# Kernel tuning notes

Measured on AMD Instinct MI355X. Metric: run time of the kernel, lower is better.

## Reference

```python
import jax, jax.numpy as jnp
import numpy as np

B, T, L, H, I, W_OUT = 64, 512, 2, 512, 128, 32


def setup_inputs() -> dict:
    key = jax.random.key(0)
    ks = jax.random.split(key, 12)
    stdv = 1.0 / np.sqrt(H)
    u = lambda k, shape: jax.random.uniform(k, shape, jnp.float32, -stdv, stdv)
    return {
        "x": jax.random.normal(ks[0], (B, T, I), jnp.float32),
        "noise": jax.random.normal(ks[1], (B, T, L, H), jnp.float32) * 0.1,
        "W_ih0": u(ks[2], (H, I)),
        "W_ih1": u(ks[3], (H, H)),
        "W_hh0": u(ks[4], (H, H)),
        "W_hh1": u(ks[5], (H, H)),
        "b_ih0": u(ks[6], (H,)),
        "b_ih1": u(ks[7], (H,)),
        "b_hh0": u(ks[8], (H,)),
        "b_hh1": u(ks[9], (H,)),
        "fc_w": u(ks[10], (W_OUT, H)),
        "fc_b": u(ks[11], (W_OUT,)),
    }


def reference(x, noise, W_ih0, W_ih1, W_hh0, W_hh1, b_ih0, b_ih1, b_hh0, b_hh1, fc_w, fc_b):
    # Sequential two-layer tanh RNN; scan over time keeps hidden state resident.
    h0 = jnp.zeros((B, H), x.dtype)
    h1 = jnp.zeros((B, H), x.dtype)

    def step(carry, inp):
        h0, h1 = carry
        x_t, n_t = inp  # x_t: [B,I], n_t: [B,L,H]
        h0 = jnp.tanh(x_t @ W_ih0.T + b_ih0 + h0 @ W_hh0.T + b_hh0 + n_t[:, 0, :])
        h1 = jnp.tanh(h0 @ W_ih1.T + b_ih1 + h1 @ W_hh1.T + b_hh1 + n_t[:, 1, :])
        return (h0, h1), None

    # time-major scan inputs
    (h0, h1), _ = jax.lax.scan(step, (h0, h1), (jnp.swapaxes(x, 0, 1), jnp.swapaxes(noise, 0, 1)))
    return h1 @ fc_w.T + fc_b  # [B, wheel_len]
```

## Files before the change

### kernel.cpp

```cpp
#include <hip/hip_runtime.h>


#define T_STEPS 512
#define NBATCH  64
#define DRING   256
#define THR_LEAD 192

typedef _Float16 half2v __attribute__((ext_vector_type(2)));

__device__ __forceinline__ unsigned pack2(float a, float b) {
    _Float16 fa = (_Float16)a, fb = (_Float16)b;
    unsigned short ua = __builtin_bit_cast(unsigned short, fa);
    unsigned short ub = __builtin_bit_cast(unsigned short, fb);
    return (unsigned)ua | ((unsigned)ub << 16);
}

__device__ __forceinline__ float dot2acc(unsigned w, unsigned h, float acc) {
#if __has_builtin(__builtin_amdgcn_fdot2)
    return __builtin_amdgcn_fdot2(__builtin_bit_cast(half2v, w),
                                  __builtin_bit_cast(half2v, h), acc, false);
#else
    half2v wv = __builtin_bit_cast(half2v, w);
    half2v hv = __builtin_bit_cast(half2v, h);
    acc = fmaf((float)wv.x, (float)hv.x, acc);
    return fmaf((float)wv.y, (float)hv.y, acc);
#endif
}

__device__ __forceinline__ float fast_tanh(float xv) {
    float e2 = __builtin_amdgcn_exp2f(xv * 2.885390082f);
    return 1.f - 2.f * __builtin_amdgcn_rcpf(e2 + 1.f);
}

__device__ __forceinline__ void bar_lgkm() {
    asm volatile("s_waitcnt lgkmcnt(0)\n\ts_barrier" ::: "memory");
}

__device__ __forceinline__ unsigned poll1(unsigned long long* p, unsigned tag,
                                          long& budget) {
    unsigned long long v = __hip_atomic_load(p, __ATOMIC_RELAXED, __HIP_MEMORY_SCOPE_AGENT);
    while ((unsigned)(v >> 32) != tag && budget > 0) {
        v = __hip_atomic_load(p, __ATOMIC_RELAXED, __HIP_MEMORY_SCOPE_AGENT);
        --budget;
    }
    return (unsigned)v;
}

#define NW0 (4 * 10 * 64 * 64)
#define NW1 (4 * 16 * 64 * 64)

__global__ void init_pack(const float* __restrict__ Wih0, const float* __restrict__ Whh0,
                          const float* __restrict__ Wih1, const float* __restrict__ Whh1,
                          unsigned* __restrict__ wp0, unsigned* __restrict__ wp1,
                          int* __restrict__ prog) {
    int gid = blockIdx.x * 256 + threadIdx.x;
    if (gid == 32) prog[32] = prog[32] + 1;
    if (gid < 32) prog[gid] = 0;
    if (gid < NW0) {
        int lane = gid & 63, slot = (gid >> 6) & 63, t12 = gid >> 12;
        int cs = t12 % 10, s = t12 / 10;
        int rr = slot >> 5, j = slot & 31;
        int r = s * 128 + 2 * lane + rr;
        float w0, w1;
        if (cs < 6)      { int m = cs * 32 + j; int p0 = (m < s * 64) ? m : m + 64;
                           w0 = Whh0[r * 512 + 2 * p0]; w1 = Whh0[r * 512 + 2 * p0 + 1]; }
        else if (cs < 8) { int p0 = s * 64 + (cs - 6) * 32 + j;
                           w0 = Whh0[r * 512 + 2 * p0]; w1 = Whh0[r * 512 + 2 * p0 + 1]; }
        else             { int px = (cs - 8) * 32 + j;
                           w0 = Wih0[r * 128 + 2 * px]; w1 = Wih0[r * 128 + 2 * px + 1]; }
        wp0[gid] = pack2(w0, w1);
    } else if (gid < NW0 + NW1) {
        int g2 = gid - NW0;
        int lane = g2 & 63, slot = (g2 >> 6) & 63, w = (g2 >> 12) & 15, s = g2 >> 16;
        int rr = slot >> 5, j = slot & 31;
        int r = s * 128 + 2 * lane + rr;
        float w0, w1;
        if (w < 8)       { int p = w * 32 + j;
                           w0 = Wih1[r * 512 + 2 * p]; w1 = Wih1[r * 512 + 2 * p + 1]; }
        else if (w < 10) { int p1 = s * 64 + (w - 8) * 32 + j;
                           w0 = Whh1[r * 512 + 2 * p1]; w1 = Whh1[r * 512 + 2 * p1 + 1]; }
        else             { int m = (w - 10) * 32 + j; int p1 = (m < s * 64) ? m : m + 64;
                           w0 = Whh1[r * 512 + 2 * p1]; w1 = Whh1[r * 512 + 2 * p1 + 1]; }
        wp1[g2] = pack2(w0, w1);
    }
}

template <int LAYER>
__device__ __forceinline__ void run_layer(
    int b0, int s, int L, int pair,
    const float* __restrict__ x, const float* __restrict__ noise,
    const unsigned* __restrict__ wp,
    const float* __restrict__ bih, const float* __restrict__ bhh,
    unsigned long long* __restrict__ hb0, unsigned long long* __restrict__ hb1,
    int* __restrict__ prog,
    const float* __restrict__ fcw, const float* __restrict__ fcb,
    float* __restrict__ out) {
    const int w = L >> 6, lane = L & 63;
    const unsigned tagbase = ((unsigned)prog[32]) << 10;
    long budget = 2000000000L;

    int wbase;
    if constexpr (LAYER == 0) { int cs = (w < 12) ? (w >> 1) : (w - 6); wbase = (s * 10 + cs) * 64; }
    else                      { wbase = (s * 16 + w) * 64; }
    unsigned wreg[64];
#pragma unroll
    for (int i = 0; i < 64; ++i) {
        wreg[i] = wp[(size_t)(wbase + i) * 64 + lane];
        asm volatile("" : "+v"(wreg[i]));
    }

    __shared__ float psum[16][2][128];
    __shared__ __align__(16) unsigned priv[16][64];
    __shared__ __align__(16) unsigned hown[128];
    for (int i = L; i < 16 * 64; i += 1024) ((unsigned*)priv)[i] = 0u;
    if (L < 128) hown[L] = 0u;

    const bool isRed = (L < 256);
    const int bbr = L >> 7, rw = L & 127;
    const int rgl = s * 128 + rw;
    float cb = 0.f, nz = 0.f;
    if (isRed) {
        cb = bih[rgl] + bhh[rgl];
        nz = noise[(((size_t)(b0 + bbr) * T_STEPS + 0) * 2 + LAYER) * 512 + rgl];
    }
    __syncthreads();

    unsigned long long pf = 0;
    unsigned long long pfR = 0;
    float2 xf = make_float2(0.f, 0.f);
    if constexpr (LAYER == 1) {
        if (w < 8) {
            unsigned v = poll1(&hb0[((size_t)0 * NBATCH + (b0 + (lane >> 5))) * 256 +
                                    (w * 32 + (lane & 31))], tagbase + 1, budget);
            pf = ((unsigned long long)(tagbase + 1) << 32) | v;
        }
    } else {
        if (w >= 14) {
            int j = lane & 31, bbl = lane >> 5;
            int px = (w - 14) * 32 + j;
            xf = *(const float2*)(x + ((size_t)(b0 + bbl) * T_STEPS + 0) * 128 + 2 * px);
        }
    }

    int known = 0;

    for (int t = 0; t < T_STEPS; ++t) {
        const bool last = (t == T_STEPS - 1);
        __builtin_amdgcn_s_setprio(1);

        if constexpr (LAYER == 1) {
            if (w < 8) {
                const int j = lane & 31, bbl = lane >> 5;
                unsigned want = tagbase + (unsigned)t + 1;
                if ((unsigned)(pf >> 32) != want) {
                    __builtin_amdgcn_s_setprio(0);
                    unsigned v = poll1(&hb0[((size_t)(t & (DRING - 1)) * NBATCH + (b0 + bbl)) * 256 +
                                            (w * 32 + j)], want, budget);
                    pf = ((unsigned long long)want << 32) | v;
                    __builtin_amdgcn_s_setprio(1);
                }
                priv[w][j * 2 + bbl] = (unsigned)pf;
                if (!last)
                    pf = __hip_atomic_load(&hb0[((size_t)((t + 1) & (DRING - 1)) * NBATCH +
                                                 (b0 + bbl)) * 256 + (w * 32 + j)],
                                           __ATOMIC_RELAXED, __HIP_MEMORY_SCOPE_AGENT);
            } else if (w >= 10) {
                if (t > 0) {
                    const int j = lane & 31, bbl = lane >> 5;
                    int m = (w - 10) * 32 + j;
                    int p2 = (m < s * 64) ? m : m + 64;
                    unsigned want = tagbase + (unsigned)t;
                    unsigned v;
                    if ((unsigned)(pfR >> 32) == want) {
                        v = (unsigned)pfR;
                    } else {
                        __builtin_amdgcn_s_setprio(0);
                        v = poll1(&hb1[((size_t)((t - 1) & 3) * NBATCH + (b0 + bbl)) * 256 + p2],
                                  want, budget);
                        __builtin_amdgcn_s_setprio(1);
                    }
                    priv[w][j * 2 + bbl] = v;
                }
            }
        } else {
            if (w < 12) {
                if (t > 0 && lane < 32) {
                    int q = w >> 1, bbw = w & 1;
                    int m = q * 32 + lane;
                    int p2 = (m < s * 64) ? m : m + 64;
                    unsigned want = tagbase + (unsigned)t;
                    unsigned v;
                    if ((unsigned)(pfR >> 32) == want) {
                        v = (unsigned)pfR;
                    } else {
                        __builtin_amdgcn_s_setprio(0);
                        v = poll1(&hb0[((size_t)((t - 1) & (DRING - 1)) * NBATCH +
                                        (b0 + bbw)) * 256 + p2],
                                  want, budget);
                        __builtin_amdgcn_s_setprio(1);
                    }
                    priv[w][lane] = v;
                }
            } else if (w >= 14) {
                const int j = lane & 31, bbl = lane >> 5;
                priv[w][j * 2 + bbl] = pack2(xf.x, xf.y);
                if (!last) {
                    int px = (w - 14) * 32 + j;
                    xf = *(const float2*)(x + ((size_t)(b0 + bbl) * T_STEPS + (t + 1)) * 128 + 2 * px);
                }
            }
        }

        float nznext = 0.f;
        if (!last && isRed)
            nznext = noise[(((size_t)(b0 + bbr) * T_STEPS + (t + 1)) * 2 + LAYER) * 512 + rgl];

        if constexpr (LAYER == 0) {
            if (w < 12) {
                const int q = w >> 1, bbw = w & 1;
                const uint4* hq = (const uint4*)&priv[w][0];
                float ax[2] = {0.f, 0.f}, ay[2] = {0.f, 0.f};
#pragma unroll
                for (int k = 0; k < 8; ++k) {
                    uint4 v = hq[k];
#pragma unroll
                    for (int r2 = 0; r2 < 2; ++r2) {
                        ax[r2] = dot2acc(wreg[r2 * 32 + 4 * k + 0], v.x, ax[r2]);
                        ay[r2] = dot2acc(wreg[r2 * 32 + 4 * k + 1], v.y, ay[r2]);
                        ax[r2] = dot2acc(wreg[r2 * 32 + 4 * k + 2], v.z, ax[r2]);
                        ay[r2] = dot2acc(wreg[r2 * 32 + 4 * k + 3], v.w, ay[r2]);
                    }
                }
                *(float2*)&psum[q][bbw][2 * lane] =
                    make_float2(ax[0] + ay[0], ax[1] + ay[1]);
            } else {
                const uint4* hq = (w < 14) ? (const uint4*)&hown[(w - 12) * 64]
                                           : (const uint4*)&priv[w][0];
                const int pidx = (w < 14) ? (6 + (w - 12)) : (8 + (w - 14));
                float a[2][2] = {{0.f, 0.f}, {0.f, 0.f}};
                float b2[2][2] = {{0.f, 0.f}, {0.f, 0.f}};
#pragma unroll
                for (int k = 0; k < 16; ++k) {
                    uint4 v = hq[k];
                    const int j0 = 2 * k, j1 = 2 * k + 1;
#pragma unroll
                    for (int r2 = 0; r2 < 2; ++r2) {
                        a[r2][0]  = dot2acc(wreg[r2 * 32 + j0], v.x, a[r2][0]);
                        a[r2][1]  = dot2acc(wreg[r2 * 32 + j0], v.y, a[r2][1]);
                        b2[r2][0] = dot2acc(wreg[r2 * 32 + j1], v.z, b2[r2][0]);
                        b2[r2][1] = dot2acc(wreg[r2 * 32 + j1], v.w, b2[r2][1]);
                    }
                }
#pragma unroll
                for (int bb2 = 0; bb2 < 2; ++bb2)
                    *(float2*)&psum[pidx][bb2][2 * lane] =
                        make_float2(a[0][bb2] + b2[0][bb2], a[1][bb2] + b2[1][bb2]);
            }
        } else {
            const uint4* hq = (w == 8 || w == 9) ? (const uint4*)&hown[(w - 8) * 64]
                                                 : (const uint4*)&priv[w][0];
            float a[2][2] = {{0.f, 0.f}, {0.f, 0.f}};
            float b2[2][2] = {{0.f, 0.f}, {0.f, 0.f}};
#pragma unroll
            for (int k = 0; k < 16; ++k) {
                uint4 v = hq[k];
                const int j0 = 2 * k, j1 = 2 * k + 1;
#pragma unroll
                for (int r2 = 0; r2 < 2; ++r2) {
                    a[r2][0]  = dot2acc(wreg[r2 * 32 + j0], v.x, a[r2][0]);
                    a[r2][1]  = dot2acc(wreg[r2 * 32 + j0], v.y, a[r2][1]);
                    b2[r2][0] = dot2acc(wreg[r2 * 32 + j1], v.z, b2[r2][0]);
                    b2[r2][1] = dot2acc(wreg[r2 * 32 + j1], v.w, b2[r2][1]);
                }
            }
#pragma unroll
            for (int bb2 = 0; bb2 < 2; ++bb2)
                *(float2*)&psum[w][bb2][2 * lane] =
                    make_float2(a[0][bb2] + b2[0][bb2], a[1][bb2] + b2[1][bb2]);
        }

        bar_lgkm();

        if (isRed) {
            constexpr int NCH = (LAYER == 0) ? 10 : 16;
            float sum = 0.f;
#pragma unroll
            for (int ch = 0; ch < NCH; ++ch) sum += psum[ch][bbr][rw];
            float h = fast_tanh(sum + cb + nz);
            float hnb = __shfl_down(h, 1);
            if ((L & 1) == 0) {
                unsigned pv = pack2(h, hnb);
                int pr = s * 64 + (rw >> 1);
                unsigned long long atom =
                    ((unsigned long long)(tagbase + (unsigned)t + 1) << 32) |
                    (unsigned long long)pv;
                if constexpr (LAYER == 0) {
                    if (t - known > THR_LEAD) {
                        __builtin_amdgcn_s_setprio(0);
                        while (t - known > THR_LEAD && budget > 0) {
                            known = __hip_atomic_load(&prog[pair], __ATOMIC_RELAXED,
                                                      __HIP_MEMORY_SCOPE_AGENT);
                            --budget;
                        }
                        __builtin_amdgcn_s_setprio(1);
                    }
                    __hip_atomic_store(&hb0[((size_t)(t & (DRING - 1)) * NBATCH + (b0 + bbr)) * 256 + pr],
                                       atom, __ATOMIC_RELAXED, __HIP_MEMORY_SCOPE_AGENT);
                } else {
                    __hip_atomic_store(&hb1[((size_t)(t & 3) * NBATCH + (b0 + bbr)) * 256 + pr],
                                       atom, __ATOMIC_RELAXED, __HIP_MEMORY_SCOPE_AGENT);
                }
                hown[(rw >> 1) * 2 + bbr] = pv;
            }
            nz = nznext;
        }
        if constexpr (LAYER == 1) {
            if (s == 0 && L == 960 && t > 1)
                __hip_atomic_store(&prog[pair], t - 2, __ATOMIC_RELAXED,
                                   __HIP_MEMORY_SCOPE_AGENT);
        }
        bar_lgkm();
        __builtin_amdgcn_s_setprio(0);

        if (!last) {
            if constexpr (LAYER == 1) {
                if (w >= 10) {
                    const int j = lane & 31, bbl = lane >> 5;
                    int m = (w - 10) * 32 + j;
                    int p2 = (m < s * 64) ? m : m + 64;
                    pfR = __hip_atomic_load(&hb1[((size_t)(t & 3) * NBATCH + (b0 + bbl)) * 256 + p2],
                                            __ATOMIC_RELAXED, __HIP_MEMORY_SCOPE_AGENT);
                }
            } else {
                if (w < 12 && lane < 32) {
                    int q = w >> 1, bbw = w & 1;
                    int m = q * 32 + lane;
                    int p2 = (m < s * 64) ? m : m + 64;
                    pfR = __hip_atomic_load(&hb0[((size_t)(t & (DRING - 1)) * NBATCH +
                                                  (b0 + bbw)) * 256 + p2],
                                            __ATOMIC_RELAXED, __HIP_MEMORY_SCOPE_AGENT);
                }
            }
        }
    }

    if constexpr (LAYER == 1) {
        if (s == 0) {
            __shared__ float hs[2][512];
            __shared__ float part[2][512];
            if (L < 512) {
                int bl = L >> 8, pr = L & 255;
                unsigned v = poll1(&hb1[((size_t)((T_STEPS - 1) & 3) * NBATCH + (b0 + bl)) * 256 + pr],
                                   tagbase + (unsigned)T_STEPS, budget);
                half2v h2 = __builtin_bit_cast(half2v, v);
                hs[bl][2 * pr] = (float)h2.x; hs[bl][2 * pr + 1] = (float)h2.y;
            }
            __syncthreads();
            {
                int bl = L >> 9, rest = L & 511, o = rest & 31, seg = rest >> 5;
                const float* wr = fcw + o * 512 + seg * 32;
                const float* hr = &hs[bl][seg * 32];
                float a = 0.f;
#pragma unroll
                for (int k = 0; k < 32; ++k) a = fmaf(wr[k], hr[k], a);
                part[bl][rest] = a;
            }
            __syncthreads();
            if (L < 64) {
                int bl = L >> 5, o = L & 31;
                float ssum = fcb[o];
#pragma unroll
                for (int sgi = 0; sgi < 16; ++sgi) ssum += part[bl][sgi * 32 + o];
                out[(b0 + bl) * 32 + o] = ssum;
            }
        }
    }
}

__global__ __launch_bounds__(1024, 4)
void rnn_dual(const float* __restrict__ x, const float* __restrict__ noise,
              const unsigned* __restrict__ wp0, const unsigned* __restrict__ wp1,
              const float* __restrict__ bih0, const float* __restrict__ bhh0,
              const float* __restrict__ bih1, const float* __restrict__ bhh1,
              const float* __restrict__ fcw, const float* __restrict__ fcb,
              unsigned long long* __restrict__ hb0,
              unsigned long long* __restrict__ hb1,
              int* __restrict__ prog,
              float* __restrict__ out) {
    const int L = threadIdx.x;
    const int gid = blockIdx.x;
    const int cl = gid & 63;
    const int s = gid >> 6;
    const int layer = cl >> 5;
    const int pair = cl & 31;
    const int b0 = pair * 2;
    if (layer == 0)
        run_layer<0>(b0, s, L, pair, x, noise, wp0, bih0, bhh0,
                     hb0, hb1, prog, nullptr, nullptr, nullptr);
    else
        run_layer<1>(b0, s, L, pair, x, noise, wp1, bih1, bhh1,
                     hb0, hb1, prog, fcw, fcb, out);
}

extern "C" void kernel_launch(void* const* d_in, const int* in_sizes, int n_in,
                              void* d_out, int out_size, void* d_ws, size_t ws_size,
                              hipStream_t stream) {
    const float* x     = (const float*)d_in[0];
    const float* noise = (const float*)d_in[1];
    const float* Wih0  = (const float*)d_in[2];
    const float* Wih1  = (const float*)d_in[3];
    const float* Whh0  = (const float*)d_in[4];
    const float* Whh1  = (const float*)d_in[5];
    const float* bih0  = (const float*)d_in[6];
    const float* bih1  = (const float*)d_in[7];
    const float* bhh0  = (const float*)d_in[8];
    const float* bhh1  = (const float*)d_in[9];
    const float* fcw   = (const float*)d_in[10];
    const float* fcb   = (const float*)d_in[11];
    float* out = (float*)d_out;

    char* ws = (char*)d_ws;
    size_t o = 0;
    unsigned* wp0 = (unsigned*)(ws + o); o += (size_t)NW0 * 4;
    unsigned* wp1 = (unsigned*)(ws + o); o += (size_t)NW1 * 4;
    unsigned long long* hb0 = (unsigned long long*)(ws + o);
    o += (size_t)DRING * NBATCH * 256 * 8;
    unsigned long long* hb1 = (unsigned long long*)(ws + o);
    o += (size_t)4 * NBATCH * 256 * 8;
    int* prog = (int*)(ws + o); o += 33 * sizeof(int);

    const int total = NW0 + NW1;
    init_pack<<<(total + 255) / 256, 256, 0, stream>>>(Wih0, Whh0, Wih1, Whh1,
                                                       wp0, wp1, prog);
    rnn_dual<<<256, 1024, 0, stream>>>(x, noise, wp0, wp1, bih0, bhh0, bih1, bhh1,
                                       fcw, fcb, hb0, hb1, prog, out);
}
```

Before: 1.118 ms.

## Replace per-step fdot2 matvec with MFMA 16x16x32 f16 on register-resident weights

The per-timestep recurrent matvec moves from scalar fdot2 dot products over private LDS slices to MFMA 16x16x32 f16 instructions, with weights repacked into MFMA A-fragments held in registers. The hidden state is placed in a double-buffered flat LDS layout that serves as the B operand. The batch of 2 is padded into the 16-wide N dimension, and the per-wave partial sums are reduced in LDS. Double buffering lets the trailing barrier of each step be dropped. The cost is wasted MFMA columns, since only 2 of 16 are real, and an extra barrier between the MFMA and reduction phases.

```diff
diff --git a/kernel.cpp b/kernel.cpp
--- a/kernel.cpp
+++ b/kernel.cpp
@@ -7,6 +7,8 @@
 #define THR_LEAD 192
 
 typedef _Float16 half2v __attribute__((ext_vector_type(2)));
+typedef _Float16 f16x8  __attribute__((ext_vector_type(8)));
+typedef float    f32x4  __attribute__((ext_vector_type(4)));
 
 __device__ __forceinline__ unsigned pack2(float a, float b) {
     _Float16 fa = (_Float16)a, fb = (_Float16)b;
@@ -15,21 +17,14 @@
     return (unsigned)ua | ((unsigned)ub << 16);
 }
 
-__device__ __forceinline__ float dot2acc(unsigned w, unsigned h, float acc) {
-#if __has_builtin(__builtin_amdgcn_fdot2)
-    return __builtin_amdgcn_fdot2(__builtin_bit_cast(half2v, w),
-                                  __builtin_bit_cast(half2v, h), acc, false);
-#else
-    half2v wv = __builtin_bit_cast(half2v, w);
-    half2v hv = __builtin_bit_cast(half2v, h);
-    acc = fmaf((float)wv.x, (float)hv.x, acc);
-    return fmaf((float)wv.y, (float)hv.y, acc);
-#endif
-}
-
 __device__ __forceinline__ float fast_tanh(float xv) {
     float e2 = __builtin_amdgcn_exp2f(xv * 2.885390082f);
     return 1.f - 2.f * __builtin_amdgcn_rcpf(e2 + 1.f);
+}
+
+__device__ __forceinline__ f32x4 mfma16(uint4 a, uint4 b, f32x4 c) {
+    return __builtin_amdgcn_mfma_f32_16x16x32_f16(
+        __builtin_bit_cast(f16x8, a), __builtin_bit_cast(f16x8, b), c, 0, 0, 0);
 }
 
 __device__ __forceinline__ void bar_lgkm() {
@@ -46,42 +41,50 @@
     return (unsigned)v;
 }
 
-#define NW0 (4 * 10 * 64 * 64)
-#define NW1 (4 * 16 * 64 * 64)
+#define NWPF (4 * 16 * 16 * 64)
 
 __global__ void init_pack(const float* __restrict__ Wih0, const float* __restrict__ Whh0,
                           const float* __restrict__ Wih1, const float* __restrict__ Whh1,
-                          unsigned* __restrict__ wp0, unsigned* __restrict__ wp1,
+                          uint4* __restrict__ wp0, uint4* __restrict__ wp1,
                           int* __restrict__ prog) {
     int gid = blockIdx.x * 256 + threadIdx.x;
     if (gid == 32) prog[32] = prog[32] + 1;
     if (gid < 32) prog[gid] = 0;
-    if (gid < NW0) {
-        int lane = gid & 63, slot = (gid >> 6) & 63, t12 = gid >> 12;
-        int cs = t12 % 10, s = t12 / 10;
-        int rr = slot >> 5, j = slot & 31;
-        int r = s * 128 + 2 * lane + rr;
-        float w0, w1;
-        if (cs < 6)      { int m = cs * 32 + j; int p0 = (m < s * 64) ? m : m + 64;
-                           w0 = Whh0[r * 512 + 2 * p0]; w1 = Whh0[r * 512 + 2 * p0 + 1]; }
-        else if (cs < 8) { int p0 = s * 64 + (cs - 6) * 32 + j;
-                           w0 = Whh0[r * 512 + 2 * p0]; w1 = Whh0[r * 512 + 2 * p0 + 1]; }
-        else             { int px = (cs - 8) * 32 + j;
-                           w0 = Wih0[r * 128 + 2 * px]; w1 = Wih0[r * 128 + 2 * px + 1]; }
-        wp0[gid] = pack2(w0, w1);
-    } else if (gid < NW0 + NW1) {
-        int g2 = gid - NW0;
-        int lane = g2 & 63, slot = (g2 >> 6) & 63, w = (g2 >> 12) & 15, s = g2 >> 16;
-        int rr = slot >> 5, j = slot & 31;
-        int r = s * 128 + 2 * lane + rr;
-        float w0, w1;
-        if (w < 8)       { int p = w * 32 + j;
-                           w0 = Wih1[r * 512 + 2 * p]; w1 = Wih1[r * 512 + 2 * p + 1]; }
-        else if (w < 10) { int p1 = s * 64 + (w - 8) * 32 + j;
-                           w0 = Whh1[r * 512 + 2 * p1]; w1 = Whh1[r * 512 + 2 * p1 + 1]; }
-        else             { int m = (w - 10) * 32 + j; int p1 = (m < s * 64) ? m : m + 64;
-                           w0 = Whh1[r * 512 + 2 * p1]; w1 = Whh1[r * 512 + 2 * p1 + 1]; }
-        wp1[g2] = pack2(w0, w1);
+    if (gid < NWPF) {
+        int lane = gid & 63, f = (gid >> 6) & 15, w = (gid >> 10) & 15, s = gid >> 14;
+        uint4 o = make_uint4(0, 0, 0, 0);
+        if (f < 10) {
+            int kc = w >> 2, rg = w & 3, j = f / 5, ktl = f % 5;
+            int r = s * 128 + (rg * 2 + j) * 16 + (lane & 15);
+            unsigned dv[4];
+#pragma unroll
+            for (int d = 0; d < 4; ++d) {
+                int kp = kc * 80 + ktl * 16 + ((lane >> 4) * 4) + d;
+                float w0, w1;
+                if (kp < 64) { w0 = Wih0[r * 128 + 2 * kp]; w1 = Wih0[r * 128 + 2 * kp + 1]; }
+                else { int p0 = kp - 64;
+                       w0 = Whh0[r * 512 + 2 * p0]; w1 = Whh0[r * 512 + 2 * p0 + 1]; }
+                dv[d] = pack2(w0, w1);
+            }
+            o = make_uint4(dv[0], dv[1], dv[2], dv[3]);
+        }
+        wp0[gid] = o;
+    } else if (gid < 2 * NWPF) {
+        int idx = gid - NWPF;
+        int lane = idx & 63, f = (idx >> 6) & 15, w = (idx >> 10) & 15, s = idx >> 14;
+        int kc = w >> 1, rg = w & 1, j = f >> 2, ktl = f & 3;
+        int r = s * 128 + (rg * 4 + j) * 16 + (lane & 15);
+        unsigned dv[4];
+#pragma unroll
+        for (int d = 0; d < 4; ++d) {
+            int kp = kc * 64 + ktl * 16 + ((lane >> 4) * 4) + d;
+            float w0, w1;
+            if (kp < 256) { w0 = Wih1[r * 512 + 2 * kp]; w1 = Wih1[r * 512 + 2 * kp + 1]; }
+            else { int p1 = kp - 256;
+                   w0 = Whh1[r * 512 + 2 * p1]; w1 = Whh1[r * 512 + 2 * p1 + 1]; }
+            dv[d] = pack2(w0, w1);
+        }
+        wp1[idx] = make_uint4(dv[0], dv[1], dv[2], dv[3]);
     }
 }
 
@@ -89,31 +92,34 @@
 __device__ __forceinline__ void run_layer(
     int b0, int s, int L, int pair,
     const float* __restrict__ x, const float* __restrict__ noise,
-    const unsigned* __restrict__ wp,
+    const uint4* __restrict__ wp,
     const float* __restrict__ bih, const float* __restrict__ bhh,
     unsigned long long* __restrict__ hb0, unsigned long long* __restrict__ hb1,
     int* __restrict__ prog,
     const float* __restrict__ fcw, const float* __restrict__ fcb,
     float* __restrict__ out) {
+    constexpr int KC    = (LAYER == 0) ? 4 : 8;
+    constexpr int KT    = (LAYER == 0) ? 5 : 4;
+    constexpr int RT    = (LAYER == 0) ? 2 : 4;
+    constexpr int NPAIR = (LAYER == 0) ? 320 : 512;
+    constexpr int OWNB  = (LAYER == 0) ? 64 : 256;
+    constexpr int NF    = (LAYER == 0) ? 10 : 16;
+    constexpr int KCP   = (LAYER == 0) ? 80 : 64;
+
     const int w = L >> 6, lane = L & 63;
     const unsigned tagbase = ((unsigned)prog[32]) << 10;
     long budget = 2000000000L;
 
-    int wbase;
-    if constexpr (LAYER == 0) { int cs = (w < 12) ? (w >> 1) : (w - 6); wbase = (s * 10 + cs) * 64; }
-    else                      { wbase = (s * 16 + w) * 64; }
-    unsigned wreg[64];
-#pragma unroll
-    for (int i = 0; i < 64; ++i) {
-        wreg[i] = wp[(size_t)(wbase + i) * 64 + lane];
-        asm volatile("" : "+v"(wreg[i]));
-    }
-
-    __shared__ float psum[16][2][128];
-    __shared__ __align__(16) unsigned priv[16][64];
-    __shared__ __align__(16) unsigned hown[128];
-    for (int i = L; i < 16 * 64; i += 1024) ((unsigned*)priv)[i] = 0u;
-    if (L < 128) hown[L] = 0u;
+    uint4 wfr[NF];
+#pragma unroll
+    for (int f = 0; f < NF; ++f) {
+        wfr[f] = wp[(size_t)(((s * 16 + w) * 16) + f) * 64 + lane];
+        asm volatile("" : "+v"(wfr[f].x), "+v"(wfr[f].y), "+v"(wfr[f].z), "+v"(wfr[f].w));
+    }
+
+    __shared__ __align__(16) unsigned hflat[2][2][NPAIR];
+    __shared__ __align__(16) float psum[2][KC][2][128];
+    for (int i = L; i < 2 * 2 * NPAIR; i += 1024) ((unsigned*)hflat)[i] = 0u;
 
     const bool isRed = (L < 256);
     const int bbr = L >> 7, rw = L & 127;
@@ -128,23 +134,20 @@
     unsigned long long pf = 0;
     unsigned long long pfR = 0;
     float2 xf = make_float2(0.f, 0.f);
-    if constexpr (LAYER == 1) {
-        if (w < 8) {
-            unsigned v = poll1(&hb0[((size_t)0 * NBATCH + (b0 + (lane >> 5))) * 256 +
-                                    (w * 32 + (lane & 31))], tagbase + 1, budget);
-            pf = ((unsigned long long)(tagbase + 1) << 32) | v;
-        }
-    } else {
+    if constexpr (LAYER == 0) {
         if (w >= 14) {
-            int j = lane & 31, bbl = lane >> 5;
-            int px = (w - 14) * 32 + j;
+            int j = lane & 31, bbl = lane >> 5, px = (w - 14) * 32 + j;
             xf = *(const float2*)(x + ((size_t)(b0 + bbl) * T_STEPS + 0) * 128 + 2 * px);
         }
     }
 
     int known = 0;
+    const int colm = lane & 15, kg = lane >> 4;
+    const int kcv = (LAYER == 0) ? (w >> 2) : (w >> 1);
+    const int rg  = (LAYER == 0) ? (w & 3)  : (w & 1);
 
     for (int t = 0; t < T_STEPS; ++t) {
+        const int p = t & 1;
         const bool last = (t == T_STEPS - 1);
         __builtin_amdgcn_s_setprio(1);
 
@@ -159,7 +162,7 @@
                     pf = ((unsigned long long)want << 32) | v;
                     __builtin_amdgcn_s_setprio(1);
                 }
-                priv[w][j * 2 + bbl] = (unsigned)pf;
+                hflat[p][bbl][w * 32 + j] = (unsigned)pf;
                 if (!last)
                     pf = __hip_atomic_load(&hb0[((size_t)((t + 1) & (DRING - 1)) * NBATCH +
                                                  (b0 + bbl)) * 256 + (w * 32 + j)],
@@ -171,43 +174,40 @@
                     int p2 = (m < s * 64) ? m : m + 64;
                     unsigned want = tagbase + (unsigned)t;
                     unsigned v;
-                    if ((unsigned)(pfR >> 32) == want) {
-                        v = (unsigned)pfR;
-                    } else {
+                    if ((unsigned)(pfR >> 32) == want) v = (unsigned)pfR;
+                    else {
                         __builtin_amdgcn_s_setprio(0);
                         v = poll1(&hb1[((size_t)((t - 1) & 3) * NBATCH + (b0 + bbl)) * 256 + p2],
                                   want, budget);
                         __builtin_amdgcn_s_setprio(1);
                     }
-                    priv[w][j * 2 + bbl] = v;
+                    hflat[p][bbl][256 + p2] = v;
                 }
             }
         } else {
-            if (w < 12) {
-                if (t > 0 && lane < 32) {
-                    int q = w >> 1, bbw = w & 1;
-                    int m = q * 32 + lane;
+            if (w >= 8 && w < 14) {
+                if (t > 0) {
+                    int idx = (w - 8) * 64 + lane;
+                    int bbl = (idx >= 192) ? 1 : 0;
+                    int m = idx - bbl * 192;
                     int p2 = (m < s * 64) ? m : m + 64;
                     unsigned want = tagbase + (unsigned)t;
                     unsigned v;
-                    if ((unsigned)(pfR >> 32) == want) {
-                        v = (unsigned)pfR;
-                    } else {
+                    if ((unsigned)(pfR >> 32) == want) v = (unsigned)pfR;
+                    else {
                         __builtin_amdgcn_s_setprio(0);
                         v = poll1(&hb0[((size_t)((t - 1) & (DRING - 1)) * NBATCH +
-                                        (b0 + bbw)) * 256 + p2],
+                                        (b0 + bbl)) * 256 + p2],
                                   want, budget);
                         __builtin_amdgcn_s_setprio(1);
                     }
-                    priv[w][lane] = v;
+                    hflat[p][bbl][64 + p2] = v;
                 }
             } else if (w >= 14) {
-                const int j = lane & 31, bbl = lane >> 5;
-                priv[w][j * 2 + bbl] = pack2(xf.x, xf.y);
-                if (!last) {
-                    int px = (w - 14) * 32 + j;
+                const int j = lane & 31, bbl = lane >> 5, px = (w - 14) * 32 + j;
+                hflat[p][bbl][px] = pack2(xf.x, xf.y);
+                if (!last)
                     xf = *(const float2*)(x + ((size_t)(b0 + bbl) * T_STEPS + (t + 1)) * 128 + 2 * px);
-                }
             }
         }
 
@@ -215,77 +215,31 @@
         if (!last && isRed)
             nznext = noise[(((size_t)(b0 + bbr) * T_STEPS + (t + 1)) * 2 + LAYER) * 512 + rgl];
 
-        if constexpr (LAYER == 0) {
-            if (w < 12) {
-                const int q = w >> 1, bbw = w & 1;
-                const uint4* hq = (const uint4*)&priv[w][0];
-                float ax[2] = {0.f, 0.f}, ay[2] = {0.f, 0.f};
-#pragma unroll
-                for (int k = 0; k < 8; ++k) {
-                    uint4 v = hq[k];
-#pragma unroll
-                    for (int r2 = 0; r2 < 2; ++r2) {
-                        ax[r2] = dot2acc(wreg[r2 * 32 + 4 * k + 0], v.x, ax[r2]);
-                        ay[r2] = dot2acc(wreg[r2 * 32 + 4 * k + 1], v.y, ay[r2]);
-                        ax[r2] = dot2acc(wreg[r2 * 32 + 4 * k + 2], v.z, ax[r2]);
-                        ay[r2] = dot2acc(wreg[r2 * 32 + 4 * k + 3], v.w, ay[r2]);
-                    }
-                }
-                *(float2*)&psum[q][bbw][2 * lane] =
-                    make_float2(ax[0] + ay[0], ax[1] + ay[1]);
-            } else {
-                const uint4* hq = (w < 14) ? (const uint4*)&hown[(w - 12) * 64]
-                                           : (const uint4*)&priv[w][0];
-                const int pidx = (w < 14) ? (6 + (w - 12)) : (8 + (w - 14));
-                float a[2][2] = {{0.f, 0.f}, {0.f, 0.f}};
-                float b2[2][2] = {{0.f, 0.f}, {0.f, 0.f}};
-#pragma unroll
-                for (int k = 0; k < 16; ++k) {
-                    uint4 v = hq[k];
-                    const int j0 = 2 * k, j1 = 2 * k + 1;
-#pragma unroll
-                    for (int r2 = 0; r2 < 2; ++r2) {
-                        a[r2][0]  = dot2acc(wreg[r2 * 32 + j0], v.x, a[r2][0]);
-                        a[r2][1]  = dot2acc(wreg[r2 * 32 + j0], v.y, a[r2][1]);
-                        b2[r2][0] = dot2acc(wreg[r2 * 32 + j1], v.z, b2[r2][0]);
-                        b2[r2][1] = dot2acc(wreg[r2 * 32 + j1], v.w, b2[r2][1]);
-                    }
-                }
-#pragma unroll
-                for (int bb2 = 0; bb2 < 2; ++bb2)
-                    *(float2*)&psum[pidx][bb2][2 * lane] =
-                        make_float2(a[0][bb2] + b2[0][bb2], a[1][bb2] + b2[1][bb2]);
-            }
-        } else {
-            const uint4* hq = (w == 8 || w == 9) ? (const uint4*)&hown[(w - 8) * 64]
-                                                 : (const uint4*)&priv[w][0];
-            float a[2][2] = {{0.f, 0.f}, {0.f, 0.f}};
-            float b2[2][2] = {{0.f, 0.f}, {0.f, 0.f}};
-#pragma unroll
-            for (int k = 0; k < 16; ++k) {
-                uint4 v = hq[k];
-                const int j0 = 2 * k, j1 = 2 * k + 1;
-#pragma unroll
-                for (int r2 = 0; r2 < 2; ++r2) {
-                    a[r2][0]  = dot2acc(wreg[r2 * 32 + j0], v.x, a[r2][0]);
-                    a[r2][1]  = dot2acc(wreg[r2 * 32 + j0], v.y, a[r2][1]);
-                    b2[r2][0] = dot2acc(wreg[r2 * 32 + j1], v.z, b2[r2][0]);
-                    b2[r2][1] = dot2acc(wreg[r2 * 32 + j1], v.w, b2[r2][1]);
-                }
-            }
-#pragma unroll
-            for (int bb2 = 0; bb2 < 2; ++bb2)
-                *(float2*)&psum[w][bb2][2 * lane] =
-                    make_float2(a[0][bb2] + b2[0][bb2], a[1][bb2] + b2[1][bb2]);
-        }
-
         bar_lgkm();
 
+        {
+            uint4 Bfr[KT];
+            const unsigned* hbase = &hflat[p][colm & 1][kcv * KCP + kg * 4];
+#pragma unroll
+            for (int ktl = 0; ktl < KT; ++ktl)
+                Bfr[ktl] = *(const uint4*)&hbase[ktl * 16];
+#pragma unroll
+            for (int j = 0; j < RT; ++j) {
+                f32x4 C = {0.f, 0.f, 0.f, 0.f};
+#pragma unroll
+                for (int ktl = 0; ktl < KT; ++ktl)
+                    C = mfma16(wfr[j * KT + ktl], Bfr[ktl], C);
+                if (colm < 2)
+                    *(f32x4*)&psum[p][kcv][colm][(rg * RT + j) * 16 + 4 * kg] = C;
+            }
+        }
+
+        bar_lgkm();
+
         if (isRed) {
-            constexpr int NCH = (LAYER == 0) ? 10 : 16;
             float sum = 0.f;
 #pragma unroll
-            for (int ch = 0; ch < NCH; ++ch) sum += psum[ch][bbr][rw];
+            for (int c2 = 0; c2 < KC; ++c2) sum += psum[p][c2][bbr][rw];
             float h = fast_tanh(sum + cb + nz);
             float hnb = __shfl_down(h, 1);
             if ((L & 1) == 0) {
@@ -310,7 +264,7 @@
                     __hip_atomic_store(&hb1[((size_t)(t & 3) * NBATCH + (b0 + bbr)) * 256 + pr],
                                        atom, __ATOMIC_RELAXED, __HIP_MEMORY_SCOPE_AGENT);
                 }
-                hown[(rw >> 1) * 2 + bbr] = pv;
+                hflat[p ^ 1][bbr][OWNB + s * 64 + (rw >> 1)] = pv;
             }
             nz = nznext;
         }
@@ -319,7 +273,6 @@
                 __hip_atomic_store(&prog[pair], t - 2, __ATOMIC_RELAXED,
                                    __HIP_MEMORY_SCOPE_AGENT);
         }
-        bar_lgkm();
         __builtin_amdgcn_s_setprio(0);
 
         if (!last) {
@@ -332,12 +285,13 @@
                                             __ATOMIC_RELAXED, __HIP_MEMORY_SCOPE_AGENT);
                 }
             } else {
-                if (w < 12 && lane < 32) {
-                    int q = w >> 1, bbw = w & 1;
-                    int m = q * 32 + lane;
+                if (w >= 8 && w < 14) {
+                    int idx = (w - 8) * 64 + lane;
+                    int bbl = (idx >= 192) ? 1 : 0;
+                    int m = idx - bbl * 192;
                     int p2 = (m < s * 64) ? m : m + 64;
                     pfR = __hip_atomic_load(&hb0[((size_t)(t & (DRING - 1)) * NBATCH +
-                                                  (b0 + bbw)) * 256 + p2],
+                                                  (b0 + bbl)) * 256 + p2],
                                             __ATOMIC_RELAXED, __HIP_MEMORY_SCOPE_AGENT);
                 }
             }
@@ -379,7 +333,7 @@
 
 __global__ __launch_bounds__(1024, 4)
 void rnn_dual(const float* __restrict__ x, const float* __restrict__ noise,
-              const unsigned* __restrict__ wp0, const unsigned* __restrict__ wp1,
+              const uint4* __restrict__ wp0, const uint4* __restrict__ wp1,
               const float* __restrict__ bih0, const float* __restrict__ bhh0,
               const float* __restrict__ bih1, const float* __restrict__ bhh1,
               const float* __restrict__ fcw, const float* __restrict__ fcb,
@@ -421,15 +375,15 @@
 
     char* ws = (char*)d_ws;
     size_t o = 0;
-    unsigned* wp0 = (unsigned*)(ws + o); o += (size_t)NW0 * 4;
-    unsigned* wp1 = (unsigned*)(ws + o); o += (size_t)NW1 * 4;
+    uint4* wp0 = (uint4*)(ws + o); o += (size_t)NWPF * 16;
+    uint4* wp1 = (uint4*)(ws + o); o += (size_t)NWPF * 16;
     unsigned long long* hb0 = (unsigned long long*)(ws + o);
     o += (size_t)DRING * NBATCH * 256 * 8;
     unsigned long long* hb1 = (unsigned long long*)(ws + o);
     o += (size_t)4 * NBATCH * 256 * 8;
     int* prog = (int*)(ws + o); o += 33 * sizeof(int);
 
-    const int total = NW0 + NW1;
+    const int total = 2 * NWPF;
     init_pack<<<(total + 255) / 256, 256, 0, stream>>>(Wih0, Whh0, Wih1, Whh1,
                                                        wp0, wp1, prog);
     rnn_dual<<<256, 1024, 0, stream>>>(x, noise, wp0, wp1, bih0, bhh0, bih1, bhh1,
```

Measured after the change: 1.123 ms. Within noise of the previous version (+0.4%).
